# Kernel optimization log

Hardware: AMD Instinct MI355X
Metric: run time of the kernel (lower is better)

## Reference

```python
import jax, jax.numpy as jnp
import numpy as np

D_IN = 1024
D_OUT = 1024
N_HEADS = 16
HEAD_DIM = D_OUT // N_HEADS
B = 2
S = 2048


def setup_inputs() -> dict:
    key = jax.random.key(0)
    ks = jax.random.split(key, 6)
    scale = 0.02
    x = jax.random.normal(ks[0], (B, S, D_IN), dtype=jnp.float32)
    # torch nn.Linear stores weight as [out, in]; y = x @ W.T + b
    Wq = jax.random.normal(ks[1], (D_OUT, D_IN), dtype=jnp.float32) * scale
    Wk = jax.random.normal(ks[2], (D_OUT, D_IN), dtype=jnp.float32) * scale
    Wv = jax.random.normal(ks[3], (D_OUT, D_IN), dtype=jnp.float32) * scale
    Wo = jax.random.normal(ks[4], (D_OUT, D_OUT), dtype=jnp.float32) * scale
    bo = jax.random.normal(ks[5], (D_OUT,), dtype=jnp.float32) * scale
    return {"x": x, "Wq": Wq, "Wk": Wk, "Wv": Wv, "Wo": Wo, "bo": bo}


def reference(x, Wq, Wk, Wv, Wo, bo):
    b, n, _ = x.shape
    # projections (no qkv bias)
    q = jnp.einsum('bnd,ed->bne', x, Wq).reshape(b, n, N_HEADS, HEAD_DIM).transpose(0, 2, 1, 3)
    k = jnp.einsum('bnd,ed->bne', x, Wk).reshape(b, n, N_HEADS, HEAD_DIM).transpose(0, 2, 1, 3)
    v = jnp.einsum('bnd,ed->bne', x, Wv).reshape(b, n, N_HEADS, HEAD_DIM).transpose(0, 2, 1, 3)
    # scores [b, h, s, s]
    scores = jnp.einsum('bhqd,bhkd->bhqk', q, k) / jnp.sqrt(jnp.float32(HEAD_DIM))
    causal = jnp.tril(jnp.ones((n, n), dtype=bool))
    scores = jnp.where(causal, scores, -jnp.inf)
    attn = jax.nn.softmax(scores, axis=-1)  # dropout p=0 -> identity
    ctx = jnp.einsum('bhqk,bhkd->bhqd', attn, v)
    ctx = ctx.transpose(0, 2, 1, 3).reshape(b, n, D_OUT)
    out = jnp.einsum('bnd,ed->bne', ctx, Wo) + bo
    return out
```

## Files before the change

kernel.cpp:

```cpp
#include <hip/hip_runtime.h>

typedef unsigned short u16;
typedef unsigned int u32;
typedef short bf16x8 __attribute__((ext_vector_type(8)));
typedef short bf16x4 __attribute__((ext_vector_type(4)));
typedef float f32x4 __attribute__((ext_vector_type(4)));
typedef u32 u32x2 __attribute__((ext_vector_type(2)));

#define LOG2E 1.4426950408889634f
#define QSCALE (0.125f * LOG2E)

__device__ __forceinline__ u16 f2b(float f) {
  u32 u = __builtin_bit_cast(u32, f);
  u32 r = (u + 0x7FFFu + ((u >> 16) & 1u)) >> 16;
  return (u16)r;
}

template <bool F32>
__device__ __forceinline__ bf16x8 load8(const void* base, size_t idx) {
  if (F32) {
    const float* p = (const float*)base + idx;
    const f32x4 a = *(const f32x4*)p;
    const f32x4 b = *(const f32x4*)(p + 4);
    bf16x8 r = { (short)f2b(a[0]), (short)f2b(a[1]), (short)f2b(a[2]),
                 (short)f2b(a[3]), (short)f2b(b[0]), (short)f2b(b[1]),
                 (short)f2b(b[2]), (short)f2b(b[3]) };
    return r;
  }
  return *(const bf16x8*)((const u16*)base + idx);
}

__device__ __forceinline__ void gl_lds16(const u16* g, u16* l) {
  __builtin_amdgcn_global_load_lds(
      (const __attribute__((address_space(1))) u32*)(const void*)g,
      (__attribute__((address_space(3))) u32*)(void*)l, 16, 0, 0);
}

__global__ __launch_bounds__(256) void convert_qw_kernel(
    const float* __restrict__ x, const float* __restrict__ wq,
    const float* __restrict__ wk, const float* __restrict__ wv,
    u16* __restrict__ xb, u16* __restrict__ wb) {
  const int i = blockIdx.x * 256 + threadIdx.x;
  if (i >= 917504) return;
  const float* src;
  u16* dst;
  size_t off;
  if (i < 524288) {
    src = x; dst = xb; off = (size_t)i * 8;
  } else {
    const int j = i - 524288;
    const int mat = j >> 17, r = j & 131071;
    src = (mat == 0) ? wq : ((mat == 1) ? wk : wv);
    dst = wb + (size_t)mat * 1048576u;
    off = (size_t)r * 8;
  }
  *(bf16x8*)(dst + off) = load8<true>(src, off);
}

__global__ __launch_bounds__(256) void convert_wo_kernel(
    const float* __restrict__ wo, u16* __restrict__ wob) {
  const int i = blockIdx.x * 256 + threadIdx.x;
  if (i >= 131072) return;
  const size_t off = (size_t)i * 8;
  *(bf16x8*)(wob + off) = load8<true>(wo, off);
}

template <bool AF32, bool WF32>
__device__ __forceinline__ void gemm_core(const void* A, const void* W,
                                          int m0, int n0, int tid,
                                          u16* As, u16* Bs,
                                          f32x4 (&acc)[4][4]) {
  const int lane = tid & 63, wave = tid >> 6;
  const int wr = wave >> 1, wc = wave & 1;
  const int l15 = lane & 15, quad = lane >> 4;
  const int r0 = tid >> 2;
  const int c8 = (tid & 3) << 3;

  const size_t ia0 = (size_t)(m0 + r0) * 1024 + c8;
  const size_t ia1 = ia0 + (size_t)64 * 1024;
  const size_t iw0 = (size_t)(n0 + r0) * 1024 + c8;
  const size_t iw1 = iw0 + (size_t)64 * 1024;

  u16* sa0 = As + r0 * 40 + c8;
  u16* sa1 = sa0 + 64 * 40;
  u16* sb0 = Bs + r0 * 40 + c8;
  u16* sb1 = sb0 + 64 * 40;

  const u16* ar = As + (wr * 64 + l15) * 40 + quad * 8;
  const u16* br = Bs + (wc * 64 + l15) * 40 + quad * 8;

  bf16x8 ra0 = load8<AF32>(A, ia0);
  bf16x8 ra1 = load8<AF32>(A, ia1);
  bf16x8 rw0 = load8<WF32>(W, iw0);
  bf16x8 rw1 = load8<WF32>(W, iw1);

  for (int k0 = 0; k0 < 1024; k0 += 32) {
    *(bf16x8*)sa0 = ra0;
    *(bf16x8*)sa1 = ra1;
    *(bf16x8*)sb0 = rw0;
    *(bf16x8*)sb1 = rw1;
    __syncthreads();
    if (k0 + 32 < 1024) {
      ra0 = load8<AF32>(A, ia0 + k0 + 32);
      ra1 = load8<AF32>(A, ia1 + k0 + 32);
      rw0 = load8<WF32>(W, iw0 + k0 + 32);
      rw1 = load8<WF32>(W, iw1 + k0 + 32);
    }
    bf16x8 af[4], bfr[4];
#pragma unroll
    for (int i = 0; i < 4; ++i) af[i] = *(const bf16x8*)(ar + i * 16 * 40);
#pragma unroll
    for (int i = 0; i < 4; ++i) bfr[i] = *(const bf16x8*)(br + i * 16 * 40);
#pragma unroll
    for (int mt = 0; mt < 4; ++mt)
#pragma unroll
      for (int nt = 0; nt < 4; ++nt)
        acc[mt][nt] = __builtin_amdgcn_mfma_f32_16x16x32_bf16(
            af[mt], bfr[nt], acc[mt][nt], 0, 0, 0);
    __syncthreads();
  }
}

__global__ __launch_bounds__(256, 2) void gemm_qkv_kernel(
    const u16* __restrict__ xb, const u16* __restrict__ wb,
    u16* __restrict__ qo, u16* __restrict__ ko, u16* __restrict__ vt) {
  __shared__ __align__(16) u16 As[128 * 40];
  __shared__ __align__(16) u16 Bs[128 * 40];
  const int tid = threadIdx.x;
  const int m0 = blockIdx.x * 128;
  const int mat = blockIdx.y >> 3;
  const int n0 = (blockIdx.y & 7) * 128;
  const u16* W = wb + (size_t)mat * 1048576u;

  f32x4 acc[4][4] = {};
  gemm_core<false, false>(xb, W, m0, n0, tid, As, Bs, acc);

  const int lane = tid & 63, wave = tid >> 6;
  const int wr = wave >> 1, wc = wave & 1;
  const int l15 = lane & 15, quad = lane >> 4;

  if (mat < 2) {
    u16* out = (mat == 0) ? qo : ko;
    const float sc = (mat == 0) ? QSCALE : 1.0f;
#pragma unroll
    for (int mt = 0; mt < 4; ++mt) {
      const int gr = m0 + wr * 64 + mt * 16 + quad * 4;
#pragma unroll
      for (int nt = 0; nt < 4; ++nt) {
        const int gc = n0 + wc * 64 + nt * 16 + l15;
#pragma unroll
        for (int r = 0; r < 4; ++r)
          out[(size_t)(gr + r) * 1024 + gc] = f2b(acc[mt][nt][r] * sc);
      }
    }
  } else {
#pragma unroll
    for (int mt = 0; mt < 4; ++mt) {
      const int gr = m0 + wr * 64 + mt * 16 + quad * 4;
      const int b = gr >> 11;
      const int s = gr & 2047;
#pragma unroll
      for (int nt = 0; nt < 4; ++nt) {
        const int gc = n0 + wc * 64 + nt * 16 + l15;
        bf16x4 pk = { (short)f2b(acc[mt][nt][0]), (short)f2b(acc[mt][nt][1]),
                      (short)f2b(acc[mt][nt][2]), (short)f2b(acc[mt][nt][3]) };
        *(bf16x4*)&vt[(size_t)(b * 1024 + gc) * 2048 + s] = pk;
      }
    }
  }
}

__global__ __launch_bounds__(256, 2) void gemm_out_kernel(
    const u16* __restrict__ ctx, const u16* __restrict__ wob,
    const float* __restrict__ bo, float* __restrict__ out) {
  __shared__ __align__(16) u16 As[128 * 40];
  __shared__ __align__(16) u16 Bs[128 * 40];
  const int tid = threadIdx.x;
  const int m0 = blockIdx.x * 128;
  const int n0 = blockIdx.y * 128;

  f32x4 acc[4][4] = {};
  gemm_core<false, false>(ctx, wob, m0, n0, tid, As, Bs, acc);

  const int lane = tid & 63, wave = tid >> 6;
  const int wr = wave >> 1, wc = wave & 1;
  const int l15 = lane & 15, quad = lane >> 4;
#pragma unroll
  for (int nt = 0; nt < 4; ++nt) {
    const int gc = n0 + wc * 64 + nt * 16 + l15;
    const float bv = bo[gc];
#pragma unroll
    for (int mt = 0; mt < 4; ++mt) {
      const int gr = m0 + wr * 64 + mt * 16 + quad * 4;
#pragma unroll
      for (int r = 0; r < 4; ++r)
        out[(size_t)(gr + r) * 1024 + gc] = acc[mt][nt][r] + bv;
    }
  }
}

__global__ __launch_bounds__(256, 4) void flash_kernel(
    const u16* q, const u16* __restrict__ k,
    const u16* __restrict__ vt, u16* ctx) {
  __shared__ __align__(16) u16 Ks[2][4096];
  __shared__ __align__(16) u16 Vs[2][4096];
  __shared__ __align__(16) u16 plds_all[4][1024];

  const int tid = threadIdx.x;
  const int wave = tid >> 6, lane = tid & 63;
  const int l15 = lane & 15, quad = lane >> 4;
  const int q0b = (31 - (int)blockIdx.x) * 64;
  const int ntiles = 32 - (int)blockIdx.x;
  const int bh = blockIdx.y;
  const int b = bh >> 4, h = bh & 15;
  const int m = q0b + wave * 16 + l15;

  const u16* qrow = q + ((size_t)(b * 2048 + m) * 1024 + h * 64);
  const bf16x8 qf0 = *(const bf16x8*)(qrow + quad * 8);
  const bf16x8 qf1 = *(const bf16x8*)(qrow + 32 + quad * 8);

  const int sr = wave * 16 + (lane >> 3);
  const int csrc = (((lane & 7) ^ ((lane >> 3) & 7)) << 3);
  const u16* kg = k + (size_t)(b * 2048) * 1024 + h * 64;
  const u16* vg = vt + (size_t)(b * 1024 + h * 64) * 2048;
  u16* plds = plds_all[wave];
  const int swz = (l15 & 7);

  f32x4 o[4] = {};
  float m_run = -INFINITY, l_lane = 0.0f;

#pragma unroll
  for (int i = 0; i < 2; ++i) {
    const int r = sr + i * 8;
    gl_lds16(kg + (size_t)r * 1024 + csrc, &Ks[0][wave * 1024 + i * 512]);
    gl_lds16(vg + (size_t)r * 2048 + csrc, &Vs[0][wave * 1024 + i * 512]);
  }
  __syncthreads();

  int buf = 0;
  for (int t = 0; t < ntiles; ++t) {
    const int n0 = t * 64;
    if (t + 1 < ntiles) {
      const int n1 = n0 + 64;
      const int nb = buf ^ 1;
#pragma unroll
      for (int i = 0; i < 2; ++i) {
        const int r = sr + i * 8;
        gl_lds16(kg + (size_t)(n1 + r) * 1024 + csrc,
                 &Ks[nb][wave * 1024 + i * 512]);
        gl_lds16(vg + (size_t)r * 2048 + n1 + csrc,
                 &Vs[nb][wave * 1024 + i * 512]);
      }
    }

    f32x4 st[4];
#pragma unroll
    for (int s4 = 0; s4 < 4; ++s4) {
      const u16* kr = &Ks[buf][(s4 * 16 + l15) * 64];
      const bf16x8 kf0 = *(const bf16x8*)(kr + ((quad ^ swz) << 3));
      const bf16x8 kf1 = *(const bf16x8*)(kr + (((4 | quad) ^ swz) << 3));
      f32x4 a = {};
      a = __builtin_amdgcn_mfma_f32_16x16x32_bf16(kf0, qf0, a, 0, 0, 0);
      a = __builtin_amdgcn_mfma_f32_16x16x32_bf16(kf1, qf1, a, 0, 0, 0);
      st[s4] = a;
    }

    float s[16];
#pragma unroll
    for (int s4 = 0; s4 < 4; ++s4)
#pragma unroll
      for (int r = 0; r < 4; ++r) s[s4 * 4 + r] = st[s4][r];
    if (t == ntiles - 1) {
#pragma unroll
      for (int s4 = 0; s4 < 4; ++s4)
#pragma unroll
        for (int r = 0; r < 4; ++r) {
          const int kv = n0 + s4 * 16 + quad * 4 + r;
          if (kv > m) s[s4 * 4 + r] = -INFINITY;
        }
    }
    float t8[8], t4[4];
#pragma unroll
    for (int i = 0; i < 8; ++i) t8[i] = fmaxf(s[i], s[i + 8]);
#pragma unroll
    for (int i = 0; i < 4; ++i) t4[i] = fmaxf(t8[i], t8[i + 4]);
    float mx = fmaxf(fmaxf(t4[0], t4[1]), fmaxf(t4[2], t4[3]));
    mx = fmaxf(mx, __shfl_xor(mx, 16));
    mx = fmaxf(mx, __shfl_xor(mx, 32));

    float mbase;
    if (__all(mx <= m_run + 8.0f)) {
      mbase = m_run;
    } else {
      mbase = fmaxf(m_run, mx);
      const float alpha = exp2f(m_run - mbase);
      l_lane *= alpha;
#pragma unroll
      for (int dt = 0; dt < 4; ++dt) o[dt] *= alpha;
      m_run = mbase;
    }

    float p[16];
#pragma unroll
    for (int i = 0; i < 16; ++i) p[i] = exp2f(s[i] - mbase);
    float u8[8], u4[4];
#pragma unroll
    for (int i = 0; i < 8; ++i) u8[i] = p[i] + p[i + 8];
#pragma unroll
    for (int i = 0; i < 4; ++i) u4[i] = u8[i] + u8[i + 4];
    l_lane += (u4[0] + u4[1]) + (u4[2] + u4[3]);

#pragma unroll
    for (int s4 = 0; s4 < 4; ++s4) {
      u32 c0, c1;
      asm("v_cvt_pk_bf16_f32 %0, %1, %2"
          : "=v"(c0) : "v"(p[s4 * 4 + 0]), "v"(p[s4 * 4 + 1]));
      asm("v_cvt_pk_bf16_f32 %0, %1, %2"
          : "=v"(c1) : "v"(p[s4 * 4 + 2]), "v"(p[s4 * 4 + 3]));
      const int wchunk = ((s4 * 2 + (quad >> 1)) ^ swz) << 3;
      u32x2 w = { c0, c1 };
      *(u32x2*)&plds[l15 * 64 + wchunk + ((quad & 1) << 2)] = w;
    }
    asm volatile("s_waitcnt lgkmcnt(0)" ::: "memory");

#pragma unroll
    for (int ks = 0; ks < 2; ++ks) {
      const bf16x8 pf =
          *(const bf16x8*)&plds[l15 * 64 + (((ks * 4 + quad) ^ swz) << 3)];
#pragma unroll
      for (int dt = 0; dt < 4; ++dt) {
        const u16* vr = &Vs[buf][(dt * 16 + l15) * 64];
        const bf16x8 vf =
            *(const bf16x8*)(vr + ((((ks << 2) | quad) ^ swz) << 3));
        o[dt] = __builtin_amdgcn_mfma_f32_16x16x32_bf16(vf, pf, o[dt], 0, 0, 0);
      }
    }

    __syncthreads();
    buf ^= 1;
  }

  float l = l_lane;
  l += __shfl_xor(l, 16);
  l += __shfl_xor(l, 32);
  const float inv = 1.0f / l;
  u16* crow = ctx + ((size_t)(b * 2048 + m) * 1024 + h * 64);
#pragma unroll
  for (int dt = 0; dt < 4; ++dt) {
    bf16x4 ov = { (short)f2b(o[dt][0] * inv), (short)f2b(o[dt][1] * inv),
                  (short)f2b(o[dt][2] * inv), (short)f2b(o[dt][3] * inv) };
    *(bf16x4*)&crow[dt * 16 + quad * 4] = ov;
  }
}

extern "C" void kernel_launch(void* const* d_in, const int* in_sizes, int n_in,
                              void* d_out, int out_size, void* d_ws,
                              size_t ws_size, hipStream_t stream) {
  const float* x  = (const float*)d_in[0];
  const float* wq = (const float*)d_in[1];
  const float* wk = (const float*)d_in[2];
  const float* wv = (const float*)d_in[3];
  const float* wo = (const float*)d_in[4];
  const float* bo = (const float*)d_in[5];
  float* out = (float*)d_out;

  u16* qb = (u16*)d_ws;
  u16* kb = qb + 4194304u;
  u16* vt = kb + 4194304u;
  u16* ctx = qb;

  u16* xb = (u16*)d_out;
  u16* wb = xb + 4194304u;
  u16* wob = kb;

  convert_qw_kernel<<<3584, 256, 0, stream>>>(x, wq, wk, wv, xb, wb);
  gemm_qkv_kernel<<<dim3(32, 24), 256, 0, stream>>>(xb, wb, qb, kb, vt);
  flash_kernel<<<dim3(32, 32), 256, 0, stream>>>(qb, kb, vt, ctx);
  convert_wo_kernel<<<512, 256, 0, stream>>>(wo, wob);
  gemm_out_kernel<<<dim3(32, 8), 256, 0, stream>>>(ctx, wob, bo, out);
}
```

Baseline: 210.7 us.

## Use direct global-to-LDS loads with XOR swizzle in GEMMs; remap flash grid per XCD

The GEMM core no longer stages tiles through registers into padded LDS. It uses global_load_lds 16-byte transfers into an unpadded, XOR-swizzled LDS tile, which shrinks shared memory and raises the occupancy hint to 3 blocks. The flash kernel moves to a 1D grid whose index is decoded so that each XCD handles a fixed set of batch-heads, with causal tile order alternating between heads to balance load and improve L2 locality. The price is that the GEMM loses its register prefetch overlap: each iteration now loads and then waits at a barrier before computing, with no double buffering.

```diff
diff --git a/kernel.cpp b/kernel.cpp
--- a/kernel.cpp
+++ b/kernel.cpp
@@ -16,18 +16,13 @@
   return (u16)r;
 }
 
-template <bool F32>
-__device__ __forceinline__ bf16x8 load8(const void* base, size_t idx) {
-  if (F32) {
-    const float* p = (const float*)base + idx;
-    const f32x4 a = *(const f32x4*)p;
-    const f32x4 b = *(const f32x4*)(p + 4);
-    bf16x8 r = { (short)f2b(a[0]), (short)f2b(a[1]), (short)f2b(a[2]),
-                 (short)f2b(a[3]), (short)f2b(b[0]), (short)f2b(b[1]),
-                 (short)f2b(b[2]), (short)f2b(b[3]) };
-    return r;
-  }
-  return *(const bf16x8*)((const u16*)base + idx);
+__device__ __forceinline__ bf16x8 cvt8(const float* p) {
+  const f32x4 a = *(const f32x4*)p;
+  const f32x4 b = *(const f32x4*)(p + 4);
+  bf16x8 r = { (short)f2b(a[0]), (short)f2b(a[1]), (short)f2b(a[2]),
+               (short)f2b(a[3]), (short)f2b(b[0]), (short)f2b(b[1]),
+               (short)f2b(b[2]), (short)f2b(b[3]) };
+  return r;
 }
 
 __device__ __forceinline__ void gl_lds16(const u16* g, u16* l) {
@@ -54,7 +49,7 @@
     dst = wb + (size_t)mat * 1048576u;
     off = (size_t)r * 8;
   }
-  *(bf16x8*)(dst + off) = load8<true>(src, off);
+  *(bf16x8*)(dst + off) = cvt8(src + off);
 }
 
 __global__ __launch_bounds__(256) void convert_wo_kernel(
@@ -62,70 +57,55 @@
   const int i = blockIdx.x * 256 + threadIdx.x;
   if (i >= 131072) return;
   const size_t off = (size_t)i * 8;
-  *(bf16x8*)(wob + off) = load8<true>(wo, off);
-}
-
-template <bool AF32, bool WF32>
-__device__ __forceinline__ void gemm_core(const void* A, const void* W,
-                                          int m0, int n0, int tid,
-                                          u16* As, u16* Bs,
-                                          f32x4 (&acc)[4][4]) {
+  *(bf16x8*)(wob + off) = cvt8(wo + off);
+}
+
+__device__ __forceinline__ void gemm_core2(const u16* A, const u16* W,
+                                           int m0, int n0, int tid,
+                                           u16* As, u16* Bs,
+                                           f32x4 (&acc)[4][4]) {
   const int lane = tid & 63, wave = tid >> 6;
   const int wr = wave >> 1, wc = wave & 1;
   const int l15 = lane & 15, quad = lane >> 4;
-  const int r0 = tid >> 2;
-  const int c8 = (tid & 3) << 3;
-
-  const size_t ia0 = (size_t)(m0 + r0) * 1024 + c8;
-  const size_t ia1 = ia0 + (size_t)64 * 1024;
-  const size_t iw0 = (size_t)(n0 + r0) * 1024 + c8;
-  const size_t iw1 = iw0 + (size_t)64 * 1024;
-
-  u16* sa0 = As + r0 * 40 + c8;
-  u16* sa1 = sa0 + 64 * 40;
-  u16* sb0 = Bs + r0 * 40 + c8;
-  u16* sb1 = sb0 + 64 * 40;
-
-  const u16* ar = As + (wr * 64 + l15) * 40 + quad * 8;
-  const u16* br = Bs + (wc * 64 + l15) * 40 + quad * 8;
-
-  bf16x8 ra0 = load8<AF32>(A, ia0);
-  bf16x8 ra1 = load8<AF32>(A, ia1);
-  bf16x8 rw0 = load8<WF32>(W, iw0);
-  bf16x8 rw1 = load8<WF32>(W, iw1);
+
+  const int srow = wave * 16 + (lane >> 2);
+  const int csrc =
+      (((lane & 3) ^ ((lane >> 2) & 3) ^ ((lane >> 4) & 3)) << 3);
+  const u16* ga = A + (size_t)(m0 + srow) * 1024 + csrc;
+  const u16* gw = W + (size_t)(n0 + srow) * 1024 + csrc;
+  u16* la = As + wave * 16 * 32;
+  u16* lb = Bs + wave * 16 * 32;
+
+  const int rswz = (l15 & 3) ^ ((l15 >> 2) & 3);
+  const u16* ar = As + (wr * 64 + l15) * 32 + ((quad ^ rswz) << 3);
+  const u16* br = Bs + (wc * 64 + l15) * 32 + ((quad ^ rswz) << 3);
 
   for (int k0 = 0; k0 < 1024; k0 += 32) {
-    *(bf16x8*)sa0 = ra0;
-    *(bf16x8*)sa1 = ra1;
-    *(bf16x8*)sb0 = rw0;
-    *(bf16x8*)sb1 = rw1;
     __syncthreads();
-    if (k0 + 32 < 1024) {
-      ra0 = load8<AF32>(A, ia0 + k0 + 32);
-      ra1 = load8<AF32>(A, ia1 + k0 + 32);
-      rw0 = load8<WF32>(W, iw0 + k0 + 32);
-      rw1 = load8<WF32>(W, iw1 + k0 + 32);
-    }
+    gl_lds16(ga + k0, la);
+    gl_lds16(ga + k0 + (size_t)64 * 1024, la + 64 * 32);
+    gl_lds16(gw + k0, lb);
+    gl_lds16(gw + k0 + (size_t)64 * 1024, lb + 64 * 32);
+    __syncthreads();
     bf16x8 af[4], bfr[4];
 #pragma unroll
-    for (int i = 0; i < 4; ++i) af[i] = *(const bf16x8*)(ar + i * 16 * 40);
-#pragma unroll
-    for (int i = 0; i < 4; ++i) bfr[i] = *(const bf16x8*)(br + i * 16 * 40);
+    for (int i = 0; i < 4; ++i) af[i] = *(const bf16x8*)(ar + i * 16 * 32);
+#pragma unroll
+    for (int i = 0; i < 4; ++i) bfr[i] = *(const bf16x8*)(br + i * 16 * 32);
 #pragma unroll
     for (int mt = 0; mt < 4; ++mt)
 #pragma unroll
       for (int nt = 0; nt < 4; ++nt)
         acc[mt][nt] = __builtin_amdgcn_mfma_f32_16x16x32_bf16(
             af[mt], bfr[nt], acc[mt][nt], 0, 0, 0);
-    __syncthreads();
-  }
-}
-
-__global__ __launch_bounds__(256, 2) void gemm_qkv_kernel(
+  }
+}
+
+__global__ __launch_bounds__(256, 3) void gemm_qkv_kernel(
     const u16* __restrict__ xb, const u16* __restrict__ wb,
     u16* __restrict__ qo, u16* __restrict__ ko, u16* __restrict__ vt) {
-  __shared__ __align__(16) u16 As[128 * 40];
-  __shared__ __align__(16) u16 Bs[128 * 40];
+  __shared__ __align__(16) u16 As[128 * 32];
+  __shared__ __align__(16) u16 Bs[128 * 32];
   const int tid = threadIdx.x;
   const int m0 = blockIdx.x * 128;
   const int mat = blockIdx.y >> 3;
@@ -133,7 +113,7 @@
   const u16* W = wb + (size_t)mat * 1048576u;
 
   f32x4 acc[4][4] = {};
-  gemm_core<false, false>(xb, W, m0, n0, tid, As, Bs, acc);
+  gemm_core2(xb, W, m0, n0, tid, As, Bs, acc);
 
   const int lane = tid & 63, wave = tid >> 6;
   const int wr = wave >> 1, wc = wave & 1;
@@ -170,17 +150,17 @@
   }
 }
 
-__global__ __launch_bounds__(256, 2) void gemm_out_kernel(
+__global__ __launch_bounds__(256, 3) void gemm_out_kernel(
     const u16* __restrict__ ctx, const u16* __restrict__ wob,
     const float* __restrict__ bo, float* __restrict__ out) {
-  __shared__ __align__(16) u16 As[128 * 40];
-  __shared__ __align__(16) u16 Bs[128 * 40];
+  __shared__ __align__(16) u16 As[128 * 32];
+  __shared__ __align__(16) u16 Bs[128 * 32];
   const int tid = threadIdx.x;
   const int m0 = blockIdx.x * 128;
   const int n0 = blockIdx.y * 128;
 
   f32x4 acc[4][4] = {};
-  gemm_core<false, false>(ctx, wob, m0, n0, tid, As, Bs, acc);
+  gemm_core2(ctx, wob, m0, n0, tid, As, Bs, acc);
 
   const int lane = tid & 63, wave = tid >> 6;
   const int wr = wave >> 1, wc = wave & 1;
@@ -209,9 +189,16 @@
   const int tid = threadIdx.x;
   const int wave = tid >> 6, lane = tid & 63;
   const int l15 = lane & 15, quad = lane >> 4;
-  const int q0b = (31 - (int)blockIdx.x) * 64;
-  const int ntiles = 32 - (int)blockIdx.x;
-  const int bh = blockIdx.y;
+
+  const int g = blockIdx.x;
+  const int xcd = g & 7;
+  const int s = g >> 3;
+  const int bh_local = s >> 5;
+  const int c = s & 31;
+  const int qv = (bh_local & 1) ? (31 - c) : c;
+  const int q0b = qv * 64;
+  const int ntiles = qv + 1;
+  const int bh = xcd + 8 * bh_local;
   const int b = bh >> 4, h = bh & 15;
   const int m = q0b + wave * 16 + l15;
 
@@ -375,7 +362,7 @@
 
   convert_qw_kernel<<<3584, 256, 0, stream>>>(x, wq, wk, wv, xb, wb);
   gemm_qkv_kernel<<<dim3(32, 24), 256, 0, stream>>>(xb, wb, qb, kb, vt);
-  flash_kernel<<<dim3(32, 32), 256, 0, stream>>>(qb, kb, vt, ctx);
+  flash_kernel<<<1024, 256, 0, stream>>>(qb, kb, vt, ctx);
   convert_wo_kernel<<<512, 256, 0, stream>>>(wo, wob);
   gemm_out_kernel<<<dim3(32, 8), 256, 0, stream>>>(ctx, wob, bo, out);
 }
```

Measured after the change: 191.7 us. 1.1x faster.
